# Kernel tuning notes

Hardware: AMD Instinct MI355X
Metric: run time of the kernel (lower is better)

## Reference

```python
import jax, jax.numpy as jnp
import numpy as np

D_MODEL = 1024
NUM_HEADS = 16
D_K = D_MODEL // NUM_HEADS
B, S = 4, 2048
NEG = -1e10


def setup_inputs() -> dict:
    key = jax.random.key(0)
    ks = jax.random.split(key, 12)
    sc = 1.0 / np.sqrt(D_MODEL)
    inp = {
        "q": jax.random.normal(ks[0], (B, S, D_MODEL), jnp.float32),
        "k": jax.random.normal(ks[1], (B, S, D_MODEL), jnp.float32),
        "v": jax.random.normal(ks[2], (B, S, D_MODEL), jnp.float32),
        "mask": jnp.broadcast_to(jnp.tril(jnp.ones((S, S), jnp.int32)), (B, 1, S, S)),
        "w_q": jax.random.normal(ks[3], (D_MODEL, D_MODEL), jnp.float32) * sc,
        "b_q": jax.random.normal(ks[4], (D_MODEL,), jnp.float32) * 0.02,
        "w_k": jax.random.normal(ks[5], (D_MODEL, D_MODEL), jnp.float32) * sc,
        "b_k": jax.random.normal(ks[6], (D_MODEL,), jnp.float32) * 0.02,
        "w_v": jax.random.normal(ks[7], (D_MODEL, D_MODEL), jnp.float32) * sc,
        "b_v": jax.random.normal(ks[8], (D_MODEL,), jnp.float32) * 0.02,
        "w_o": jax.random.normal(ks[9], (D_MODEL, D_MODEL), jnp.float32) * sc,
        "b_o": jax.random.normal(ks[10], (D_MODEL,), jnp.float32) * 0.02,
    }
    return inp


def reference(q, k, v, mask, w_q, b_q, w_k, b_k, w_v, b_v, w_o, b_o):
    b = q.shape[0]
    split = lambda x: x.reshape(b, -1, NUM_HEADS, D_K).transpose(0, 2, 1, 3)  # [B,H,S,d_k]
    Q = split(q @ w_q.T + b_q)
    K = split(k @ w_k.T + b_k)
    V = split(v @ w_v.T + b_v)
    energy = jnp.einsum("bhqd,bhkd->bhqk", Q, K) / jnp.sqrt(jnp.float32(D_K))
    energy = jnp.where(mask == 0, jnp.float32(NEG), energy)
    attn = jax.nn.softmax(energy, axis=-1)
    out = jnp.einsum("bhqk,bhkd->bhqd", attn, V)
    out = out.transpose(0, 2, 1, 3).reshape(b, -1, D_MODEL)
    return out @ w_o.T + b_o
```

## Files before the change

kernel.cpp:

```cpp
#include <hip/hip_runtime.h>

typedef unsigned short u16;
typedef unsigned int u32;
typedef short short8 __attribute__((ext_vector_type(8)));
typedef u16 u16x8 __attribute__((ext_vector_type(8)));
typedef u16 u16x4 __attribute__((ext_vector_type(4)));
typedef float f32x4 __attribute__((ext_vector_type(4)));
typedef float f32x16 __attribute__((ext_vector_type(16)));

__device__ __forceinline__ u16 f2bf(float f) {
  u32 u = __builtin_bit_cast(u32, f);
  u += 0x7fff + ((u >> 16) & 1);
  return (u16)(u >> 16);
}
__device__ __forceinline__ float ex2(float x) {
  float r; asm("v_exp_f32 %0, %1" : "=v"(r) : "v"(x)); return r;
}
__device__ __forceinline__ u32 cvtpk(float lo, float hi) {
  u32 r; asm("v_cvt_pk_bf16_f32 %0, %1, %2" : "=v"(r) : "v"(lo), "v"(hi)); return r;
}

__device__ __forceinline__ void gload16(const u16* g, u16* l) {
  __builtin_amdgcn_global_load_lds(
      (const __attribute__((address_space(1))) u32*)(unsigned long long)(const void*)g,
      (__attribute__((address_space(3))) u32*)(u32)(unsigned long long)(void*)l,
      16, 0, 0);
}

__global__ __launch_bounds__(256) void cvt3(const float* __restrict__ a, const float* __restrict__ b,
                                            const float* __restrict__ c, u16* __restrict__ oa,
                                            u16* __restrict__ ob, u16* __restrict__ oc, int n4) {
  const int z = blockIdx.y;
  const float* s = z == 0 ? a : (z == 1 ? b : c);
  u16* d = z == 0 ? oa : (z == 1 ? ob : oc);
  int i = blockIdx.x * 256 + threadIdx.x;
  if (i >= n4) return;
  float4 f = reinterpret_cast<const float4*>(s)[i];
  u16x4 o;
  o.x = f2bf(f.x); o.y = f2bf(f.y); o.z = f2bf(f.z); o.w = f2bf(f.w);
  reinterpret_cast<u16x4*>(d)[i] = o;
}

__global__ __launch_bounds__(256) void cvt4(const float* __restrict__ a, const float* __restrict__ b,
                                            const float* __restrict__ c, const float* __restrict__ d0,
                                            u16* __restrict__ oa, u16* __restrict__ ob,
                                            u16* __restrict__ oc, u16* __restrict__ od, int n4) {
  const int z = blockIdx.y;
  const float* s = z == 0 ? a : (z == 1 ? b : (z == 2 ? c : d0));
  u16* d = z == 0 ? oa : (z == 1 ? ob : (z == 2 ? oc : od));
  int i = blockIdx.x * 256 + threadIdx.x;
  if (i >= n4) return;
  float4 f = reinterpret_cast<const float4*>(s)[i];
  u16x4 o;
  o.x = f2bf(f.x); o.y = f2bf(f.y); o.z = f2bf(f.z); o.w = f2bf(f.w);
  reinterpret_cast<u16x4*>(d)[i] = o;
}

__device__ __forceinline__ void gemm_core(const u16* __restrict__ A, const u16* __restrict__ Bm,
                                          const float* __restrict__ bias, u16* __restrict__ Cb,
                                          float* __restrict__ Cf, int K, int ldc, int ccol0,
                                          float cs) {
  __shared__ __align__(16) u16 As[3][128 * 32];
  __shared__ __align__(16) u16 Bs[3][128 * 32];
  const int t = threadIdx.x, l = t & 63, w = t >> 6;
  const int lg = l >> 4, lr = l & 15;
  const int m0 = blockIdx.y * 128, n0 = blockIdx.x * 128;
  const int wr = (w >> 1) * 64, wc = (w & 1) * 64;
  const int srow = w * 32 + (l >> 2);
  const int scol = ((l & 3) ^ ((l >> 3) & 3)) * 8;
  const u16* ga = A + (size_t)(m0 + srow) * K + scol;
  const u16* gb = Bm + (size_t)(n0 + srow) * K + scol;
  const int ldst = w * 1024 + l * 8;
  const int ko = (lg ^ ((lr >> 1) & 3)) * 8;

  u16* a0 = &As[0][0]; u16* a1 = &As[1][0]; u16* a2 = &As[2][0];
  u16* b0 = &Bs[0][0]; u16* b1 = &Bs[1][0]; u16* b2 = &Bs[2][0];

  f32x4 acc[4][4];
#pragma unroll
  for (int i = 0; i < 4; ++i)
#pragma unroll
    for (int jj = 0; jj < 4; ++jj) acc[i][jj] = (f32x4){0.f, 0.f, 0.f, 0.f};

  const int ni = K >> 5;
  gload16(ga, a0 + ldst);
  gload16(ga + 16 * (size_t)K, a0 + ldst + 512);
  gload16(gb, b0 + ldst);
  gload16(gb + 16 * (size_t)K, b0 + ldst + 512);
  gload16(ga + 32, a1 + ldst);
  gload16(ga + 32 + 16 * (size_t)K, a1 + ldst + 512);
  gload16(gb + 32, b1 + ldst);
  gload16(gb + 32 + 16 * (size_t)K, b1 + ldst + 512);
  asm volatile("s_waitcnt vmcnt(4)" ::: "memory");
  __builtin_amdgcn_s_barrier();
  __builtin_amdgcn_sched_barrier(0);

  for (int it = 0; it < ni; ++it) {
    const bool pf = (it + 2) < ni;
    if (pf) {
      const int k2 = (it + 2) << 5;
      gload16(ga + k2, a2 + ldst);
      gload16(ga + k2 + 16 * (size_t)K, a2 + ldst + 512);
      gload16(gb + k2, b2 + ldst);
      gload16(gb + k2 + 16 * (size_t)K, b2 + ldst + 512);
    }
    short8 af[4], bf[4];
#pragma unroll
    for (int i = 0; i < 4; ++i)
      af[i] = *reinterpret_cast<const short8*>(&a0[(wr + 16 * i + lr) * 32 + ko]);
#pragma unroll
    for (int jj = 0; jj < 4; ++jj)
      bf[jj] = *reinterpret_cast<const short8*>(&b0[(wc + 16 * jj + lr) * 32 + ko]);
    __builtin_amdgcn_s_setprio(1);
#pragma unroll
    for (int i = 0; i < 4; ++i)
#pragma unroll
      for (int jj = 0; jj < 4; ++jj)
        acc[i][jj] = __builtin_amdgcn_mfma_f32_16x16x32_bf16(af[i], bf[jj], acc[i][jj], 0, 0, 0);
    __builtin_amdgcn_s_setprio(0);
    if (it + 1 < ni) {
      if (pf) asm volatile("s_waitcnt vmcnt(4)" ::: "memory");
      else    asm volatile("s_waitcnt vmcnt(0)" ::: "memory");
      __builtin_amdgcn_s_barrier();
      __builtin_amdgcn_sched_barrier(0);
    }
    u16* tmp;
    tmp = a0; a0 = a1; a1 = a2; a2 = tmp;
    tmp = b0; b0 = b1; b1 = b2; b2 = tmp;
  }

#pragma unroll
  for (int i = 0; i < 4; ++i) {
#pragma unroll
    for (int jj = 0; jj < 4; ++jj) {
      int col = n0 + wc + 16 * jj + lr;
      float bv = bias[col];
#pragma unroll
      for (int r = 0; r < 4; ++r) {
        int row = m0 + wr + 16 * i + lg * 4 + r;
        float val = (acc[i][jj][r] + bv) * cs;
        if (Cb) Cb[(size_t)row * ldc + ccol0 + col] = f2bf(val);
        else    Cf[(size_t)row * ldc + col] = val;
      }
    }
  }
}

#define QSCALE 0.18033688011112042f

__global__ __launch_bounds__(256) void gemm_qkv(const u16* __restrict__ Xq, const u16* __restrict__ Xk,
                                                const u16* __restrict__ Xv, const u16* __restrict__ Wq,
                                                const u16* __restrict__ Wk, const u16* __restrict__ Wv,
                                                const float* __restrict__ bq, const float* __restrict__ bk,
                                                const float* __restrict__ bv, u16* __restrict__ QKV) {
  const int z = blockIdx.z;
  const u16* A = z == 0 ? Xq : (z == 1 ? Xk : Xv);
  const u16* B = z == 0 ? Wq : (z == 1 ? Wk : Wv);
  const float* bias = z == 0 ? bq : (z == 1 ? bk : bv);
  gemm_core(A, B, bias, QKV, nullptr, 1024, 3072, z * 1024, z == 0 ? QSCALE : 1.0f);
}

__global__ __launch_bounds__(256) void gemm_out(const u16* __restrict__ AO, const u16* __restrict__ Wo,
                                                const float* __restrict__ bo, float* __restrict__ out) {
  gemm_core(AO, Wo, bo, nullptr, out, 1024, 1024, 0, 1.0f);
}

#define LDK 72
#define DEFER_THR 11.0f

__global__ __launch_bounds__(256, 4) void attn_fwd(const u16* __restrict__ QKV, u16* __restrict__ O) {
  __shared__ __align__(16) u16 Kt[64 * LDK];
  __shared__ __align__(16) u16 Vt[64 * LDK];

  const int t = threadIdx.x, l = t & 63, w = t >> 6;
  const int lq = l & 31, hi = l >> 5;
  const int bh = blockIdx.x;
  const int qb = 15 - (int)blockIdx.y;
  const int b = bh >> 4, h = bh & 15;
  const size_t rowb = (size_t)b * 2048;
  const int qcol = h * 64, kcol = 1024 + h * 64, vcol = 2048 + h * 64;
  const int q0w = qb * 128 + 32 * w;
  const int nt = 2 * qb + 2;

  short8 qf[4];
  {
    const u16* qp = QKV + (rowb + q0w + lq) * 3072 + qcol + hi * 8;
#pragma unroll
    for (int ks = 0; ks < 4; ++ks) qf[ks] = *reinterpret_cast<const short8*>(qp + ks * 16);
  }

  f32x16 oa[2];
#pragma unroll
  for (int dt = 0; dt < 2; ++dt)
#pragma unroll
    for (int r = 0; r < 16; ++r) oa[dt][r] = 0.f;
  float m_run = -1e30f, l_run = 0.f;

  const int kr = t & 31, kc = (t >> 5) * 8;
  short8 ka0, ka1;
  u16x8 va0, va1;

  auto stage_load = [&](int kv64) {
    const u16* kp = QKV + (rowb + (size_t)kv64 * 64 + kr) * 3072 + kcol + kc;
    ka0 = *reinterpret_cast<const short8*>(kp);
    ka1 = *reinterpret_cast<const short8*>(kp + 32 * 3072);
    const u16* vp = QKV + (rowb + (size_t)kv64 * 64 + 2 * kr) * 3072 + vcol + kc;
    va0 = *reinterpret_cast<const u16x8*>(vp);
    va1 = *reinterpret_cast<const u16x8*>(vp + 3072);
  };
  auto stage_write = [&]() {
    *reinterpret_cast<short8*>(&Kt[kr * LDK + kc]) = ka0;
    *reinterpret_cast<short8*>(&Kt[(kr + 32) * LDK + kc]) = ka1;
#pragma unroll
    for (int jj = 0; jj < 8; ++jj) {
      u32 pk = (u32)va0[jj] | ((u32)va1[jj] << 16);
      *reinterpret_cast<u32*>(&Vt[(kc + jj) * LDK + 2 * kr]) = pk;
    }
  };

  auto flash = [&](int kv0) {
    short8 kf[4], vf[4];
    const int kt32 = (kv0 & 63);
#pragma unroll
    for (int ks = 0; ks < 4; ++ks)
      kf[ks] = *reinterpret_cast<const short8*>(&Kt[(kt32 + lq) * LDK + ks * 16 + hi * 8]);
#pragma unroll
    for (int dt = 0; dt < 2; ++dt)
#pragma unroll
      for (int ks2 = 0; ks2 < 2; ++ks2)
        vf[2 * dt + ks2] = *reinterpret_cast<const short8*>(
            &Vt[(dt * 32 + lq) * LDK + kt32 + ks2 * 16 + hi * 8]);
    f32x16 s;
#pragma unroll
    for (int r = 0; r < 16; ++r) s[r] = 0.f;
    __builtin_amdgcn_s_setprio(1);
#pragma unroll
    for (int ks = 0; ks < 4; ++ks)
      s = __builtin_amdgcn_mfma_f32_32x32x16_bf16(kf[ks], qf[ks], s, 0, 0, 0);
    __builtin_amdgcn_s_setprio(0);
    const bool diag = (kv0 == q0w);
    float p[16];
#pragma unroll
    for (int r = 0; r < 16; ++r) {
      float x = s[r];
      if (diag) {
        int off = (r & 3) + 8 * (r >> 2) + 4 * hi;
        if (off > lq) x = -1e30f;
      }
      p[r] = x;
    }
    float pm = fmaxf(fmaxf(fmaxf(p[0], p[1]), fmaxf(p[2], p[3])),
                     fmaxf(fmaxf(p[4], p[5]), fmaxf(p[6], p[7])));
    pm = fmaxf(pm, fmaxf(fmaxf(fmaxf(p[8], p[9]), fmaxf(p[10], p[11])),
                         fmaxf(fmaxf(p[12], p[13]), fmaxf(p[14], p[15]))));
    pm = fmaxf(pm, __shfl_xor(pm, 32));
    if (!__all(pm <= m_run + DEFER_THR)) {
      float mnew = fmaxf(m_run, pm);
      float al = ex2(m_run - mnew);
      l_run *= al;
#pragma unroll
      for (int dt = 0; dt < 2; ++dt)
#pragma unroll
        for (int r = 0; r < 16; ++r) oa[dt][r] *= al;
      m_run = mnew;
    }
    float ps = 0.f;
#pragma unroll
    for (int r = 0; r < 16; ++r) {
      float e = ex2(p[r] - m_run);
      p[r] = e;
      ps += e;
    }
    ps += __shfl_xor(ps, 32);
    l_run += ps;
    u32 P[8], X[8];
#pragma unroll
    for (int m2 = 0; m2 < 8; ++m2) {
      P[m2] = cvtpk(p[2 * m2], p[2 * m2 + 1]);
      X[m2] = (u32)__shfl_xor((int)P[m2], 32);
    }
    short8 pf[2];
#pragma unroll
    for (int ks2 = 0; ks2 < 2; ++ks2) {
      union { u32 u[4]; short8 v; } uu;
      uu.u[0] = hi ? X[4 * ks2 + 2] : P[4 * ks2 + 0];
      uu.u[1] = hi ? X[4 * ks2 + 3] : P[4 * ks2 + 1];
      uu.u[2] = hi ? P[4 * ks2 + 2] : X[4 * ks2 + 0];
      uu.u[3] = hi ? P[4 * ks2 + 3] : X[4 * ks2 + 1];
      pf[ks2] = uu.v;
    }
    __builtin_amdgcn_s_setprio(1);
#pragma unroll
    for (int ks2 = 0; ks2 < 2; ++ks2)
#pragma unroll
      for (int dt = 0; dt < 2; ++dt)
        oa[dt] = __builtin_amdgcn_mfma_f32_32x32x16_bf16(vf[2 * dt + ks2], pf[ks2], oa[dt], 0, 0, 0);
    __builtin_amdgcn_s_setprio(0);
  };

  stage_load(0);
  stage_write();
  __syncthreads();

  for (int kb = 0; kb < nt; ++kb) {
    if (kb + 1 < nt) stage_load(kb + 1);
#pragma unroll
    for (int kt = 0; kt < 2; ++kt) {
      const int kv0 = kb * 64 + kt * 32;
      if (kv0 <= q0w) flash(kv0);
    }
    __syncthreads();
    if (kb + 1 < nt) stage_write();
    __syncthreads();
  }

  const float inv = __builtin_amdgcn_rcpf(l_run);
  const size_t obase = (rowb + q0w + lq) * 1024 + h * 64;
#pragma unroll
  for (int dt = 0; dt < 2; ++dt) {
    u32 Bp[8], Xb[8];
#pragma unroll
    for (int m2 = 0; m2 < 8; ++m2) {
      Bp[m2] = cvtpk(oa[dt][2 * m2] * inv, oa[dt][2 * m2 + 1] * inv);
      Xb[m2] = (u32)__shfl_xor((int)Bp[m2], 32);
    }
    if (hi == dt) {
#pragma unroll
      for (int c = 0; c < 4; ++c) {
        union { u32 u[4]; short8 v; } uu;
        uu.u[0] = hi ? Xb[2 * c]     : Bp[2 * c];
        uu.u[1] = hi ? Xb[2 * c + 1] : Bp[2 * c + 1];
        uu.u[2] = hi ? Bp[2 * c]     : Xb[2 * c];
        uu.u[3] = hi ? Bp[2 * c + 1] : Xb[2 * c + 1];
        *reinterpret_cast<short8*>(&O[obase + dt * 32 + c * 8]) = uu.v;
      }
    }
  }
}

extern "C" void kernel_launch(void* const* d_in, const int* in_sizes, int n_in,
                              void* d_out, int out_size, void* d_ws, size_t ws_size,
                              hipStream_t stream) {
  const float* q  = (const float*)d_in[0];
  const float* k  = (const float*)d_in[1];
  const float* v  = (const float*)d_in[2];
  const float* wq = (const float*)d_in[4];
  const float* bq = (const float*)d_in[5];
  const float* wk = (const float*)d_in[6];
  const float* bk = (const float*)d_in[7];
  const float* wv = (const float*)d_in[8];
  const float* bv = (const float*)d_in[9];
  const float* wo = (const float*)d_in[10];
  const float* bo = (const float*)d_in[11];
  float* out = (float*)d_out;

  u16* ws = (u16*)d_ws;
  const size_t NE = 8192ull * 1024;
  const size_t WE = 1024ull * 1024;
  u16* Xq   = ws;
  u16* Xk   = Xq + NE;
  u16* Xv   = Xk + NE;
  u16* Wq   = Xv + NE;
  u16* Wk   = Wq + WE;
  u16* Wv   = Wk + WE;
  u16* Wo   = Wv + WE;
  u16* QKVp = Wo + WE;
  u16* AO   = QKVp + 8192ull * 3072;

  cvt3<<<dim3(8192, 3), 256, 0, stream>>>(q, k, v, Xq, Xk, Xv, (int)(NE / 4));
  cvt4<<<dim3(1024, 4), 256, 0, stream>>>(wq, wk, wv, wo, Wq, Wk, Wv, Wo, (int)(WE / 4));

  gemm_qkv<<<dim3(8, 64, 3), 256, 0, stream>>>(Xq, Xk, Xv, Wq, Wk, Wv, bq, bk, bv, QKVp);

  attn_fwd<<<dim3(64, 16), 256, 0, stream>>>(QKVp, AO);

  gemm_out<<<dim3(8, 64), 256, 0, stream>>>(AO, Wo, bo, out);
}
```

Baseline: 373.9 us.

## Double-buffer attention K/V tiles, merge cvt kernels, use 64-row tiles for output GEMM

```diff
diff --git a/kernel.cpp b/kernel.cpp
--- a/kernel.cpp
+++ b/kernel.cpp
@@ -27,99 +27,101 @@
       16, 0, 0);
 }
 
-__global__ __launch_bounds__(256) void cvt3(const float* __restrict__ a, const float* __restrict__ b,
-                                            const float* __restrict__ c, u16* __restrict__ oa,
-                                            u16* __restrict__ ob, u16* __restrict__ oc, int n4) {
-  const int z = blockIdx.y;
-  const float* s = z == 0 ? a : (z == 1 ? b : c);
-  u16* d = z == 0 ? oa : (z == 1 ? ob : oc);
-  int i = blockIdx.x * 256 + threadIdx.x;
-  if (i >= n4) return;
+#define NB 8192
+#define WB 1024
+
+__global__ __launch_bounds__(256) void cvt_all(
+    const float* __restrict__ q, const float* __restrict__ k, const float* __restrict__ v,
+    const float* __restrict__ wq, const float* __restrict__ wk, const float* __restrict__ wv,
+    const float* __restrict__ wo, u16* __restrict__ Xq, u16* __restrict__ Xk,
+    u16* __restrict__ Xv, u16* __restrict__ Wq, u16* __restrict__ Wk, u16* __restrict__ Wv,
+    u16* __restrict__ Wo) {
+  int bid = blockIdx.x;
+  const float* s; u16* d; int x;
+  if (bid < 3 * NB) {
+    int z = bid / NB; x = bid - z * NB;
+    s = z == 0 ? q : (z == 1 ? k : v);
+    d = z == 0 ? Xq : (z == 1 ? Xk : Xv);
+  } else {
+    int r = bid - 3 * NB;
+    int z = r / WB; x = r - z * WB;
+    s = z == 0 ? wq : (z == 1 ? wk : (z == 2 ? wv : wo));
+    d = z == 0 ? Wq : (z == 1 ? Wk : (z == 2 ? Wv : Wo));
+  }
+  int i = x * 256 + threadIdx.x;
   float4 f = reinterpret_cast<const float4*>(s)[i];
   u16x4 o;
   o.x = f2bf(f.x); o.y = f2bf(f.y); o.z = f2bf(f.z); o.w = f2bf(f.w);
   reinterpret_cast<u16x4*>(d)[i] = o;
 }
 
-__global__ __launch_bounds__(256) void cvt4(const float* __restrict__ a, const float* __restrict__ b,
-                                            const float* __restrict__ c, const float* __restrict__ d0,
-                                            u16* __restrict__ oa, u16* __restrict__ ob,
-                                            u16* __restrict__ oc, u16* __restrict__ od, int n4) {
-  const int z = blockIdx.y;
-  const float* s = z == 0 ? a : (z == 1 ? b : (z == 2 ? c : d0));
-  u16* d = z == 0 ? oa : (z == 1 ? ob : (z == 2 ? oc : od));
-  int i = blockIdx.x * 256 + threadIdx.x;
-  if (i >= n4) return;
-  float4 f = reinterpret_cast<const float4*>(s)[i];
-  u16x4 o;
-  o.x = f2bf(f.x); o.y = f2bf(f.y); o.z = f2bf(f.z); o.w = f2bf(f.w);
-  reinterpret_cast<u16x4*>(d)[i] = o;
-}
-
+template <int BM>
 __device__ __forceinline__ void gemm_core(const u16* __restrict__ A, const u16* __restrict__ Bm,
                                           const float* __restrict__ bias, u16* __restrict__ Cb,
                                           float* __restrict__ Cf, int K, int ldc, int ccol0,
                                           float cs) {
-  __shared__ __align__(16) u16 As[3][128 * 32];
+  constexpr int MI = BM / 32;
+  __shared__ __align__(16) u16 As[3][BM * 32];
   __shared__ __align__(16) u16 Bs[3][128 * 32];
   const int t = threadIdx.x, l = t & 63, w = t >> 6;
   const int lg = l >> 4, lr = l & 15;
-  const int m0 = blockIdx.y * 128, n0 = blockIdx.x * 128;
-  const int wr = (w >> 1) * 64, wc = (w & 1) * 64;
-  const int srow = w * 32 + (l >> 2);
+  const int m0 = blockIdx.y * BM, n0 = blockIdx.x * 128;
+  const int wr = (w >> 1) * (16 * MI), wc = (w & 1) * 64;
+  const int srowA = (BM == 128) ? (w * 32 + (l >> 2)) : (w * 16 + (l >> 2));
+  const int srowB = w * 32 + (l >> 2);
   const int scol = ((l & 3) ^ ((l >> 3) & 3)) * 8;
-  const u16* ga = A + (size_t)(m0 + srow) * K + scol;
-  const u16* gb = Bm + (size_t)(n0 + srow) * K + scol;
-  const int ldst = w * 1024 + l * 8;
+  const u16* ga = A + (size_t)(m0 + srowA) * K + scol;
+  const u16* gb = Bm + (size_t)(n0 + srowB) * K + scol;
+  const int ldstA = (BM == 128) ? (w * 1024 + l * 8) : (w * 512 + l * 8);
+  const int ldstB = w * 1024 + l * 8;
   const int ko = (lg ^ ((lr >> 1) & 3)) * 8;
 
   u16* a0 = &As[0][0]; u16* a1 = &As[1][0]; u16* a2 = &As[2][0];
   u16* b0 = &Bs[0][0]; u16* b1 = &Bs[1][0]; u16* b2 = &Bs[2][0];
 
-  f32x4 acc[4][4];
-#pragma unroll
-  for (int i = 0; i < 4; ++i)
+  auto stage = [&](int kk, u16* ab, u16* bb) {
+    gload16(ga + kk, ab + ldstA);
+    if constexpr (BM == 128) gload16(ga + kk + 16 * (size_t)K, ab + ldstA + 512);
+    gload16(gb + kk, bb + ldstB);
+    gload16(gb + kk + 16 * (size_t)K, bb + ldstB + 512);
+  };
+  auto wait_counted = [&]() {
+    if constexpr (BM == 128) asm volatile("s_waitcnt vmcnt(4)" ::: "memory");
+    else                     asm volatile("s_waitcnt vmcnt(3)" ::: "memory");
+  };
+
+  f32x4 acc[MI][4];
+#pragma unroll
+  for (int i = 0; i < MI; ++i)
 #pragma unroll
     for (int jj = 0; jj < 4; ++jj) acc[i][jj] = (f32x4){0.f, 0.f, 0.f, 0.f};
 
   const int ni = K >> 5;
-  gload16(ga, a0 + ldst);
-  gload16(ga + 16 * (size_t)K, a0 + ldst + 512);
-  gload16(gb, b0 + ldst);
-  gload16(gb + 16 * (size_t)K, b0 + ldst + 512);
-  gload16(ga + 32, a1 + ldst);
-  gload16(ga + 32 + 16 * (size_t)K, a1 + ldst + 512);
-  gload16(gb + 32, b1 + ldst);
-  gload16(gb + 32 + 16 * (size_t)K, b1 + ldst + 512);
-  asm volatile("s_waitcnt vmcnt(4)" ::: "memory");
+  stage(0, a0, b0);
+  stage(32, a1, b1);
+  wait_counted();
   __builtin_amdgcn_s_barrier();
   __builtin_amdgcn_sched_barrier(0);
 
   for (int it = 0; it < ni; ++it) {
     const bool pf = (it + 2) < ni;
-    if (pf) {
-      const int k2 = (it + 2) << 5;
-      gload16(ga + k2, a2 + ldst);
-      gload16(ga + k2 + 16 * (size_t)K, a2 + ldst + 512);
-      gload16(gb + k2, b2 + ldst);
-      gload16(gb + k2 + 16 * (size_t)K, b2 + ldst + 512);
-    }
-    short8 af[4], bf[4];
-#pragma unroll
-    for (int i = 0; i < 4; ++i)
+    if (pf) stage((it + 2) << 5, a2, b2);
+    short8 af[MI], bf[4];
+#pragma unroll
+    for (int i = 0; i < MI; ++i)
       af[i] = *reinterpret_cast<const short8*>(&a0[(wr + 16 * i + lr) * 32 + ko]);
 #pragma unroll
     for (int jj = 0; jj < 4; ++jj)
       bf[jj] = *reinterpret_cast<const short8*>(&b0[(wc + 16 * jj + lr) * 32 + ko]);
     __builtin_amdgcn_s_setprio(1);
 #pragma unroll
-    for (int i = 0; i < 4; ++i)
+    for (int i = 0; i < MI; ++i)
 #pragma unroll
       for (int jj = 0; jj < 4; ++jj)
         acc[i][jj] = __builtin_amdgcn_mfma_f32_16x16x32_bf16(af[i], bf[jj], acc[i][jj], 0, 0, 0);
     __builtin_amdgcn_s_setprio(0);
     if (it + 1 < ni) {
-      if (pf) asm volatile("s_waitcnt vmcnt(4)" ::: "memory");
+      if (pf) wait_counted();
       else    asm volatile("s_waitcnt vmcnt(0)" ::: "memory");
       __builtin_amdgcn_s_barrier();
       __builtin_amdgcn_sched_barrier(0);
@@ -130,7 +132,7 @@
   }
 
 #pragma unroll
-  for (int i = 0; i < 4; ++i) {
+  for (int i = 0; i < MI; ++i) {
 #pragma unroll
     for (int jj = 0; jj < 4; ++jj) {
       int col = n0 + wc + 16 * jj + lr;
@@ -157,20 +159,20 @@
   const u16* A = z == 0 ? Xq : (z == 1 ? Xk : Xv);
   const u16* B = z == 0 ? Wq : (z == 1 ? Wk : Wv);
   const float* bias = z == 0 ? bq : (z == 1 ? bk : bv);
-  gemm_core(A, B, bias, QKV, nullptr, 1024, 3072, z * 1024, z == 0 ? QSCALE : 1.0f);
+  gemm_core<128>(A, B, bias, QKV, nullptr, 1024, 3072, z * 1024, z == 0 ? QSCALE : 1.0f);
 }
 
 __global__ __launch_bounds__(256) void gemm_out(const u16* __restrict__ AO, const u16* __restrict__ Wo,
                                                 const float* __restrict__ bo, float* __restrict__ out) {
-  gemm_core(AO, Wo, bo, nullptr, out, 1024, 1024, 0, 1.0f);
+  gemm_core<64>(AO, Wo, bo, nullptr, out, 1024, 1024, 0, 1.0f);
 }
 
 #define LDK 72
 #define DEFER_THR 11.0f
 
-__global__ __launch_bounds__(256, 4) void attn_fwd(const u16* __restrict__ QKV, u16* __restrict__ O) {
-  __shared__ __align__(16) u16 Kt[64 * LDK];
-  __shared__ __align__(16) u16 Vt[64 * LDK];
+__global__ __launch_bounds__(256, 3) void attn_fwd(const u16* __restrict__ QKV, u16* __restrict__ O) {
+  __shared__ __align__(16) u16 Kt[2][64 * LDK];
+  __shared__ __align__(16) u16 Vt[2][64 * LDK];
 
   const int t = threadIdx.x, l = t & 63, w = t >> 6;
   const int lq = l & 31, hi = l >> 5;
@@ -208,78 +210,23 @@
     va0 = *reinterpret_cast<const u16x8*>(vp);
     va1 = *reinterpret_cast<const u16x8*>(vp + 3072);
   };
-  auto stage_write = [&]() {
-    *reinterpret_cast<short8*>(&Kt[kr * LDK + kc]) = ka0;
-    *reinterpret_cast<short8*>(&Kt[(kr + 32) * LDK + kc]) = ka1;
+  auto stage_write = [&](int buf) {
+    *reinterpret_cast<short8*>(&Kt[buf][kr * LDK + kc]) = ka0;
+    *reinterpret_cast<short8*>(&Kt[buf][(kr + 32) * LDK + kc]) = ka1;
 #pragma unroll
     for (int jj = 0; jj < 8; ++jj) {
       u32 pk = (u32)va0[jj] | ((u32)va1[jj] << 16);
-      *reinterpret_cast<u32*>(&Vt[(kc + jj) * LDK + 2 * kr]) = pk;
-    }
-  };
-
-  auto flash = [&](int kv0) {
-    short8 kf[4], vf[4];
-    const int kt32 = (kv0 & 63);
-#pragma unroll
-    for (int ks = 0; ks < 4; ++ks)
-      kf[ks] = *reinterpret_cast<const short8*>(&Kt[(kt32 + lq) * LDK + ks * 16 + hi * 8]);
-#pragma unroll
-    for (int dt = 0; dt < 2; ++dt)
-#pragma unroll
-      for (int ks2 = 0; ks2 < 2; ++ks2)
-        vf[2 * dt + ks2] = *reinterpret_cast<const short8*>(
-            &Vt[(dt * 32 + lq) * LDK + kt32 + ks2 * 16 + hi * 8]);
-    f32x16 s;
-#pragma unroll
-    for (int r = 0; r < 16; ++r) s[r] = 0.f;
-    __builtin_amdgcn_s_setprio(1);
-#pragma unroll
-    for (int ks = 0; ks < 4; ++ks)
-      s = __builtin_amdgcn_mfma_f32_32x32x16_bf16(kf[ks], qf[ks], s, 0, 0, 0);
-    __builtin_amdgcn_s_setprio(0);
-    const bool diag = (kv0 == q0w);
-    float p[16];
-#pragma unroll
-    for (int r = 0; r < 16; ++r) {
-      float x = s[r];
-      if (diag) {
-        int off = (r & 3) + 8 * (r >> 2) + 4 * hi;
-        if (off > lq) x = -1e30f;
-      }
-      p[r] = x;
-    }
-    float pm = fmaxf(fmaxf(fmaxf(p[0], p[1]), fmaxf(p[2], p[3])),
-                     fmaxf(fmaxf(p[4], p[5]), fmaxf(p[6], p[7])));
-    pm = fmaxf(pm, fmaxf(fmaxf(fmaxf(p[8], p[9]), fmaxf(p[10], p[11])),
-                         fmaxf(fmaxf(p[12], p[13]), fmaxf(p[14], p[15]))));
-    pm = fmaxf(pm, __shfl_xor(pm, 32));
-    if (!__all(pm <= m_run + DEFER_THR)) {
-      float mnew = fmaxf(m_run, pm);
-      float al = ex2(m_run - mnew);
-      l_run *= al;
-#pragma unroll
-      for (int dt = 0; dt < 2; ++dt)
-#pragma unroll
-        for (int r = 0; r < 16; ++r) oa[dt][r] *= al;
-      m_run = mnew;
-    }
-    float ps = 0.f;
-#pragma unroll
-    for (int r = 0; r < 16; ++r) {
-      float e = ex2(p[r] - m_run);
-      p[r] = e;
-      ps += e;
-    }
-    ps += __shfl_xor(ps, 32);
-    l_run += ps;
+      *reinterpret_cast<u32*>(&Vt[buf][(kc + jj) * LDK + 2 * kr]) = pk;
+    }
+  };
+
+  auto packP = [&](const f32x16& p, short8 pf[2]) {
     u32 P[8], X[8];
 #pragma unroll
     for (int m2 = 0; m2 < 8; ++m2) {
       P[m2] = cvtpk(p[2 * m2], p[2 * m2 + 1]);
       X[m2] = (u32)__shfl_xor((int)P[m2], 32);
     }
-    short8 pf[2];
 #pragma unroll
     for (int ks2 = 0; ks2 < 2; ++ks2) {
       union { u32 u[4]; short8 v; } uu;
@@ -289,28 +236,118 @@
       uu.u[3] = hi ? P[4 * ks2 + 3] : X[4 * ks2 + 1];
       pf[ks2] = uu.v;
     }
+  };
+  auto pvStep = [&](const u16* Vtc, int kt32, const short8 pf[2]) {
     __builtin_amdgcn_s_setprio(1);
 #pragma unroll
     for (int ks2 = 0; ks2 < 2; ++ks2)
 #pragma unroll
+      for (int dt = 0; dt < 2; ++dt) {
+        short8 vf = *reinterpret_cast<const short8*>(
+            &Vtc[(dt * 32 + lq) * LDK + kt32 + ks2 * 16 + hi * 8]);
+        oa[dt] = __builtin_amdgcn_mfma_f32_32x32x16_bf16(vf, pf[ks2], oa[dt], 0, 0, 0);
+      }
+    __builtin_amdgcn_s_setprio(0);
+  };
+  auto rescale_sum = [&](float pm) {
+    if (!__all(pm <= m_run + DEFER_THR)) {
+      float mnew = fmaxf(m_run, pm);
+      float al = ex2(m_run - mnew);
+      l_run *= al;
+#pragma unroll
       for (int dt = 0; dt < 2; ++dt)
-        oa[dt] = __builtin_amdgcn_mfma_f32_32x32x16_bf16(vf[2 * dt + ks2], pf[ks2], oa[dt], 0, 0, 0);
+#pragma unroll
+        for (int r = 0; r < 16; ++r) oa[dt][r] *= al;
+      m_run = mnew;
+    }
+  };
+
+  auto flash2 = [&](const u16* Ktc, const u16* Vtc, bool diag1) {
+    f32x16 s0, s1;
+#pragma unroll
+    for (int r = 0; r < 16; ++r) { s0[r] = 0.f; s1[r] = 0.f; }
+    __builtin_amdgcn_s_setprio(1);
+#pragma unroll
+    for (int ks = 0; ks < 4; ++ks) {
+      short8 kf = *reinterpret_cast<const short8*>(&Ktc[lq * LDK + ks * 16 + hi * 8]);
+      s0 = __builtin_amdgcn_mfma_f32_32x32x16_bf16(kf, qf[ks], s0, 0, 0, 0);
+    }
+#pragma unroll
+    for (int ks = 0; ks < 4; ++ks) {
+      short8 kf = *reinterpret_cast<const short8*>(&Ktc[(32 + lq) * LDK + ks * 16 + hi * 8]);
+      s1 = __builtin_amdgcn_mfma_f32_32x32x16_bf16(kf, qf[ks], s1, 0, 0, 0);
+    }
     __builtin_amdgcn_s_setprio(0);
+    if (diag1) {
+#pragma unroll
+      for (int r = 0; r < 16; ++r) {
+        int off = (r & 3) + 8 * (r >> 2) + 4 * hi;
+        if (off > lq) s1[r] = -1e30f;
+      }
+    }
+    float pm = fmaxf(s0[0], s1[0]);
+#pragma unroll
+    for (int r = 1; r < 16; ++r) pm = fmaxf(pm, fmaxf(s0[r], s1[r]));
+    pm = fmaxf(pm, __shfl_xor(pm, 32));
+    rescale_sum(pm);
+    float ps = 0.f;
+#pragma unroll
+    for (int r = 0; r < 16; ++r) { float e = ex2(s0[r] - m_run); s0[r] = e; ps += e; }
+#pragma unroll
+    for (int r = 0; r < 16; ++r) { float e = ex2(s1[r] - m_run); s1[r] = e; ps += e; }
+    ps += __shfl_xor(ps, 32);
+    l_run += ps;
+    short8 pf[2];
+    packP(s0, pf);
+    pvStep(Vtc, 0, pf);
+    packP(s1, pf);
+    pvStep(Vtc, 32, pf);
+  };
+
+  auto flash1 = [&](const u16* Ktc, const u16* Vtc) {
+    f32x16 s;
+#pragma unroll
+    for (int r = 0; r < 16; ++r) s[r] = 0.f;
+    __builtin_amdgcn_s_setprio(1);
+#pragma unroll
+    for (int ks = 0; ks < 4; ++ks) {
+      short8 kf = *reinterpret_cast<const short8*>(&Ktc[lq * LDK + ks * 16 + hi * 8]);
+      s = __builtin_amdgcn_mfma_f32_32x32x16_bf16(kf, qf[ks], s, 0, 0, 0);
+    }
+    __builtin_amdgcn_s_setprio(0);
+#pragma unroll
+    for (int r = 0; r < 16; ++r) {
+      int off = (r & 3) + 8 * (r >> 2) + 4 * hi;
+      if (off > lq) s[r] = -1e30f;
+    }
+    float pm = s[0];
+#pragma unroll
+    for (int r = 1; r < 16; ++r) pm = fmaxf(pm, s[r]);
+    pm = fmaxf(pm, __shfl_xor(pm, 32));
+    rescale_sum(pm);
+    float ps = 0.f;
+#pragma unroll
+    for (int r = 0; r < 16; ++r) { float e = ex2(s[r] - m_run); s[r] = e; ps += e; }
+    ps += __shfl_xor(ps, 32);
+    l_run += ps;
+    short8 pf[2];
+    packP(s, pf);
+    pvStep(Vtc, 0, pf);
   };
 
   stage_load(0);
-  stage_write();
+  stage_write(0);
   __syncthreads();
 
   for (int kb = 0; kb < nt; ++kb) {
+    const int cur = kb & 1;
+    const u16* Ktc = &Kt[cur][0];
+    const u16* Vtc = &Vt[cur][0];
     if (kb + 1 < nt) stage_load(kb + 1);
-#pragma unroll
-    for (int kt = 0; kt < 2; ++kt) {
-      const int kv0 = kb * 64 + kt * 32;
-      if (kv0 <= q0w) flash(kv0);
-    }
-    __syncthreads();
-    if (kb + 1 < nt) stage_write();
+    const int rel = q0w - kb * 64;
+    if (rel >= 32)      flash2(Ktc, Vtc, rel == 32);
+    else if (rel == 0)  flash1(Ktc, Vtc);
+    if (kb + 1 < nt) stage_write(cur ^ 1);
     __syncthreads();
   }
 
@@ -367,12 +404,12 @@
   u16* QKVp = Wo + WE;
   u16* AO   = QKVp + 8192ull * 3072;
 
-  cvt3<<<dim3(8192, 3), 256, 0, stream>>>(q, k, v, Xq, Xk, Xv, (int)(NE / 4));
-  cvt4<<<dim3(1024, 4), 256, 0, stream>>>(wq, wk, wv, wo, Wq, Wk, Wv, Wo, (int)(WE / 4));
+  cvt_all<<<3 * NB + 4 * WB, 256, 0, stream>>>(q, k, v, wq, wk, wv, wo,
+                                               Xq, Xk, Xv, Wq, Wk, Wv, Wo);
 
   gemm_qkv<<<dim3(8, 64, 3), 256, 0, stream>>>(Xq, Xk, Xv, Wq, Wk, Wv, bq, bk, bv, QKVp);
 
   attn_fwd<<<dim3(64, 16), 256, 0, stream>>>(QKVp, AO);
 
-  gemm_out<<<dim3(8, 64), 256, 0, stream>>>(AO, Wo, bo, out);
-}
+  gemm_out<<<dim3(8, 128), 256, 0, stream>>>(AO, Wo, bo, out);
+}
```

New measurement: 356.9 us. 1.05x faster.
